# Optimization experiments

Hardware: AMD Instinct MI355X
Metric: run time of the kernel (lower is better)

Reference implementation:

```python
import jax, jax.numpy as jnp
import numpy as np

N_HEADS = 16
EMBED_DIM = 2048
BATCH, SEQ = 2, 2048


def setup_inputs() -> dict:
    key = jax.random.key(0)
    k1, k2, k3, k4, k5 = jax.random.split(key, 5)
    s_in = 1.0 / np.sqrt(EMBED_DIM)
    return {
        "x": jax.random.normal(k1, (BATCH, SEQ, EMBED_DIM), dtype=jnp.float32),
        "w_in": jax.random.normal(k2, (3 * EMBED_DIM, EMBED_DIM), dtype=jnp.float32) * s_in,
        "b_in": jax.random.normal(k3, (3 * EMBED_DIM,), dtype=jnp.float32) * 0.02,
        "w_out": jax.random.normal(k4, (EMBED_DIM, EMBED_DIM), dtype=jnp.float32) * s_in,
        "b_out": jax.random.normal(k5, (EMBED_DIM,), dtype=jnp.float32) * 0.02,
        "causal_mask": 1,
    }


def reference(x, w_in, b_in, w_out, b_out, causal_mask):
    b, l, e = x.shape
    h, d = N_HEADS, e // N_HEADS
    qkv = x @ w_in.T + b_in                      # [b, l, 3e]
    q, k, v = jnp.split(qkv, 3, axis=-1)
    # b l (h d) -> b h l d
    q = q.reshape(b, l, h, d).transpose(0, 2, 1, 3)
    k = k.reshape(b, l, h, d).transpose(0, 2, 1, 3)
    v = v.reshape(b, l, h, d).transpose(0, 2, 1, 3)
    scores = jnp.einsum("bhqd,bhkd->bhqk", q, k) / jnp.sqrt(jnp.float32(d))
    if causal_mask:
        tri = jnp.triu(jnp.ones((l, l), dtype=bool), k=1)  # True above diagonal
        scores = jnp.where(tri, -jnp.inf, scores)
    attn = jax.nn.softmax(scores, axis=-1)
    out = jnp.einsum("bhqk,bhkd->bhqd", attn, v)  # [b, h, l, d]
    out = out.transpose(0, 2, 1, 3).reshape(b, l, e)
    return out @ w_out.T + b_out
```

## Files before the change

### kernel.cpp

```cpp
#include <hip/hip_runtime.h>
#include <hip/hip_bf16.h>
#include <math.h>

typedef __attribute__((ext_vector_type(4))) float floatx4;
typedef __attribute__((ext_vector_type(16))) float floatx16;
typedef __attribute__((ext_vector_type(8))) __bf16 bf16x8;

__device__ __forceinline__ unsigned short f2bf(float f) {
    union { float f; unsigned int u; } v; v.f = f;
    unsigned int u = v.u;
    u += 0x7FFFu + ((u >> 16) & 1u);
    return (unsigned short)(u >> 16);
}

__device__ __forceinline__ unsigned int pkbf(float a, float b) {
    return (unsigned int)f2bf(a) | ((unsigned int)f2bf(b) << 16);
}

__device__ __forceinline__ void gl_lds16(const void* g, void* l) {
    __builtin_amdgcn_global_load_lds(
        (const __attribute__((address_space(1))) void*)g,
        (__attribute__((address_space(3))) void*)l, 16, 0, 0);
}

__global__ void cast_f32_bf16(const float* __restrict__ in,
                              unsigned short* __restrict__ out, int n) {
    int i = (blockIdx.x * blockDim.x + threadIdx.x) * 4;
    if (i + 4 <= n) {
        float4 f = *(const float4*)(in + i);
        ushort4 o;
        o.x = f2bf(f.x); o.y = f2bf(f.y); o.z = f2bf(f.z); o.w = f2bf(f.w);
        *(ushort4*)(out + i) = o;
    }
}


#define VMCNT(n) asm volatile("s_waitcnt vmcnt(" #n ")" ::: "memory")
#define LGKM0()  asm volatile("s_waitcnt lgkmcnt(0)" ::: "memory")
#define BARF()   do { asm volatile("" ::: "memory"); __builtin_amdgcn_s_barrier(); \
                      asm volatile("" ::: "memory"); } while (0)

#define STAGE_A4(bsel, tt, h) do { \
    const unsigned short* _s = Ab + (size_t)((h) * 128 + rstage) * K + (tt) * 64 + scol; \
    char* _d = bufc + (bsel) * 49152 + (h) * 16384 + wid * 1024; \
    gl_lds16(_s, _d); \
    gl_lds16(_s + (size_t)64 * K, _d + 8192); \
} while (0)

#define STAGE_B4(bsel, tt, h) do { \
    const unsigned short* _s = Bb + (size_t)((h) * 64 + rstage) * K + (tt) * 64 + scol; \
    char* _d = bufc + (bsel) * 49152 + 32768 + (h) * 8192 + wid * 1024; \
    gl_lds16(_s, _d); \
} while (0)

#define STAGE_TILE(bsel, tt) do { \
    STAGE_A4(bsel, tt, 0); STAGE_A4(bsel, tt, 1); \
    STAGE_B4(bsel, tt, 0); STAGE_B4(bsel, tt, 1); \
} while (0)

#define RDA(base, ii, kse) (*(const bf16x8*)((base) + (ii) * 2048 + rdoffA + (kse)))
#define RDB(base, jj, kse) (*(const bf16x8*)((base) + (jj) * 2048 + rdoffB + (kse)))

#define MFMA_C(iofs) do { \
    __builtin_amdgcn_s_setprio(1); \
    _Pragma("unroll") \
    for (int ii = 0; ii < 4; ++ii) { \
        _Pragma("unroll") \
        for (int jj = 0; jj < 2; ++jj) { \
            acc[(iofs) + ii][jj] = __builtin_amdgcn_mfma_f32_16x16x32_bf16( \
                aF[((iofs) + ii) * 2 + 0], bL[jj * 2 + 0], acc[(iofs) + ii][jj], 0, 0, 0); \
            acc[(iofs) + ii][jj] = __builtin_amdgcn_mfma_f32_16x16x32_bf16( \
                aF[((iofs) + ii) * 2 + 1], bL[jj * 2 + 1], acc[(iofs) + ii][jj], 0, 0, 0); \
        } } \
    __builtin_amdgcn_s_setprio(0); \
} while (0)

template<int MODE>
__global__ __launch_bounds__(512, 2) void gemm4p(
    const unsigned short* __restrict__ A,
    const unsigned short* __restrict__ B,
    const float* __restrict__ bias,
    float* __restrict__ Cf,
    unsigned short* __restrict__ q_ws,
    unsigned short* __restrict__ k_ws,
    unsigned short* __restrict__ vT_ws,
    int M, int N, int K)
{
    extern __shared__ char ldsc[];
    char* const bufc = ldsc;

    const int nby = M >> 8;
    const int nwg = gridDim.x;
    const int qq = nwg >> 3;
    const int wg = (blockIdx.x & 7) * qq + (blockIdx.x >> 3);
    const int by = wg % nby, bx = wg / nby;
    const int m0 = by << 8, n0 = bx << 7;

    const int tid = threadIdx.x;
    const int lane = tid & 63, wid = tid >> 6;
    const int li = lane & 15, quad = lane >> 4;
    const int wr = wid >> 2, wc = wid & 3;

    const int rstage = tid >> 3;
    const int scol = (((tid & 7) ^ ((tid >> 3) & 7)) << 3);
    const unsigned short* Ab = A + (size_t)m0 * K;
    const unsigned short* Bb = B + (size_t)n0 * K;

    const int swz = (lane & 7) << 4;
    const int ks0 = ((quad << 4)     ) ^ swz;
    const int ks1 = ((quad << 4) + 64) ^ swz;
    const int rdoffA = li * 128;
    const int rdoffB = li * 128 + ((wc & 1) << 12);

    const char* rdA0 = bufc + wr * 16384;
    const char* rdB0 = bufc + 32768 + (wc >> 1) * 8192;
    const char* rdA1 = rdA0 + 49152;
    const char* rdB1 = rdB0 + 49152;

    floatx4 acc[8][2] = {};
    bf16x8 aF[16], bL[4];

    const int KTn = K >> 6;

    STAGE_TILE(0, 0);
    STAGE_TILE(1, 1);
    VMCNT(6);
    BARF();

    for (int t = 0; t < KTn; t += 2) {
        const bool pf = (t + 2 < KTn);

        #pragma unroll
        for (int ii = 0; ii < 8; ++ii) { aF[ii*2+0] = RDA(rdA0, ii, ks0); aF[ii*2+1] = RDA(rdA0, ii, ks1); }
        #pragma unroll
        for (int jj = 0; jj < 2; ++jj) { bL[jj*2+0] = RDB(rdB0, jj, ks0); bL[jj*2+1] = RDB(rdB0, jj, ks1); }
        BARF();
        MFMA_C(0);
        LGKM0();
        BARF();

        if (pf) STAGE_TILE(0, t + 2);
        BARF();
        MFMA_C(4);
        if (pf) { VMCNT(6); } else { VMCNT(0); }
        BARF();

        #pragma unroll
        for (int ii = 0; ii < 8; ++ii) { aF[ii*2+0] = RDA(rdA1, ii, ks0); aF[ii*2+1] = RDA(rdA1, ii, ks1); }
        #pragma unroll
        for (int jj = 0; jj < 2; ++jj) { bL[jj*2+0] = RDB(rdB1, jj, ks0); bL[jj*2+1] = RDB(rdB1, jj, ks1); }
        BARF();
        MFMA_C(0);
        LGKM0();
        BARF();

        if (pf) STAGE_TILE(1, t + 3);
        BARF();
        MFMA_C(4);
        if (pf) { VMCNT(6); } else { VMCNT(0); }
        BARF();
    }

    const int colb = wc * 32;
    const int rowb = wr * 128;
    if (MODE == 0) {
        #pragma unroll
        for (int i2 = 0; i2 < 8; ++i2)
            #pragma unroll
            for (int j2 = 0; j2 < 2; ++j2) {
                const int col = n0 + colb + j2 * 16 + li;
                const float bv = bias[col];
                #pragma unroll
                for (int r = 0; r < 4; ++r) {
                    const int row = m0 + rowb + i2 * 16 + quad * 4 + r;
                    Cf[(size_t)row * N + col] = acc[i2][j2][r] + bv;
                }
            }
    } else {
        const int which = bx >> 4;
        const int hh = bx & 15;
        const int lbase = m0 & 2047;
        const size_t bh = (size_t)((m0 >> 11) * 16 + hh);
        if (which == 2) {
            unsigned short (*Lv)[264] = (unsigned short(*)[264])ldsc;
            #pragma unroll
            for (int i2 = 0; i2 < 8; ++i2)
                #pragma unroll
                for (int j2 = 0; j2 < 2; ++j2) {
                    const int col = colb + j2 * 16 + li;
                    const float bv = bias[n0 + col];
                    #pragma unroll
                    for (int r = 0; r < 4; ++r) {
                        const int row = rowb + i2 * 16 + quad * 4 + r;
                        Lv[col][row] = f2bf(acc[i2][j2][r] + bv);
                    }
                }
            __syncthreads();
            #pragma unroll
            for (int c = 0; c < 8; ++c) {
                int chunk = c * 512 + tid;
                int d = chunk >> 5;
                int ls = (chunk & 31) * 8;
                *(uint4*)(vT_ws + (bh * 128 + d) * 2048 + lbase + ls) =
                    *(const uint4*)&Lv[d][ls];
            }
        } else {
            unsigned short (*Lq)[136] = (unsigned short(*)[136])ldsc;
            #pragma unroll
            for (int i2 = 0; i2 < 8; ++i2)
                #pragma unroll
                for (int j2 = 0; j2 < 2; ++j2) {
                    const int col = colb + j2 * 16 + li;
                    const float bv = bias[n0 + col];
                    #pragma unroll
                    for (int r = 0; r < 4; ++r) {
                        const int row = rowb + i2 * 16 + quad * 4 + r;
                        Lq[row][col] = f2bf(acc[i2][j2][r] + bv);
                    }
                }
            __syncthreads();
            unsigned short* dst = which ? k_ws : q_ws;
            #pragma unroll
            for (int c = 0; c < 8; ++c) {
                int chunk = c * 512 + tid;
                int row = chunk >> 4;
                int dc = (chunk & 15) * 8;
                *(uint4*)(dst + (bh * 2048 + lbase + row) * (size_t)128 + dc) =
                    *(const uint4*)&Lq[row][dc];
            }
        }
    }
}

__global__ __launch_bounds__(256, 3) void attn_kernel(
    const unsigned short* __restrict__ q_ws,
    const unsigned short* __restrict__ k_ws,
    const unsigned short* __restrict__ vT_ws,
    unsigned short* __restrict__ aout,
    const int* __restrict__ causal_ptr)
{
    __shared__ unsigned short smem[64 * 136 + 128 * 72];
    unsigned short* const Ks = smem;
    unsigned short* const Vs = smem + 64 * 136;

    const int ord = blockIdx.x;
    int qt, bhid;
    if (ord < 256) { qt = ord >> 5;              bhid = ord & 31; }
    else           { qt = 15 - ((ord - 256) >> 5); bhid = ord & 31; }
    const int b = bhid >> 4, h = bhid & 15;

    const int tid = threadIdx.x;
    const int lane = tid & 63, w = tid >> 6;
    const int lq = lane & 31;
    const int half = lane >> 5;
    const size_t bh = (size_t)(b * 16 + h);
    const unsigned short* Qp = q_ws + bh * 2048 * 128;
    const unsigned short* Kp = k_ws + bh * 2048 * 128;
    const unsigned short* Vp = vT_ws + bh * 128 * 2048;
    const int causal = causal_ptr[0];
    const float scale = 0.08838834764831845f;

    const int qg = qt * 128 + w * 32 + lq;
    bf16x8 qf[8];
    #pragma unroll
    for (int s = 0; s < 8; ++s)
        qf[s] = *(const bf16x8*)(Qp + (size_t)qg * 128 + s * 16 + half * 8);

    floatx16 O[4] = {};
    float m_i = -INFINITY, l_i = 0.f;

    const int myEnd = causal ? (2 * qt + 1) : 31;
    for (int kt = 0; kt <= myEnd; ++kt) {
        #pragma unroll
        for (int c = 0; c < 4; ++c) {
            int chunk = c * 256 + tid;
            int krow = chunk >> 4;
            int kcc  = (chunk & 15) * 8;
            *(uint4*)(Ks + krow * 136 + kcc) =
                *(const uint4*)(Kp + (size_t)(kt * 64 + krow) * 128 + kcc);
            int vrow = chunk >> 3;
            int vcc  = (chunk & 7) * 8;
            *(uint4*)(Vs + vrow * 72 + vcc) =
                *(const uint4*)(Vp + (size_t)vrow * 2048 + kt * 64 + vcc);
        }
        __syncthreads();

        floatx16 S[2] = {};
        #pragma unroll
        for (int ct = 0; ct < 2; ++ct)
            #pragma unroll
            for (int s = 0; s < 8; ++s) {
                bf16x8 kf = *(const bf16x8*)(Ks + (ct * 32 + lq) * 136 + s * 16 + half * 8);
                S[ct] = __builtin_amdgcn_mfma_f32_32x32x16_bf16(kf, qf[s], S[ct], 0, 0, 0);
            }

        const bool diag = causal && (kt >= 2 * qt);
        float mx = -INFINITY;
        #pragma unroll
        for (int ct = 0; ct < 2; ++ct)
            #pragma unroll
            for (int r = 0; r < 16; ++r) {
                float sv = S[ct][r] * scale;
                if (diag) {
                    int key = kt * 64 + 32 * ct + (r & 3) + 8 * (r >> 2) + 4 * half;
                    if (key > qg) sv = -INFINITY;
                }
                S[ct][r] = sv;
                mx = fmaxf(mx, sv);
            }
        mx = fmaxf(mx, __shfl_xor(mx, 32, 64));
        float m_new = fmaxf(m_i, mx);
        float m_use = (m_new == -INFINITY) ? 0.f : m_new;
        float alpha = __expf(m_i - m_use);

        float rs = 0.f;
        #pragma unroll
        for (int ct = 0; ct < 2; ++ct)
            #pragma unroll
            for (int r = 0; r < 16; ++r) {
                float p = __expf(S[ct][r] - m_use);
                S[ct][r] = p;
                rs += p;
            }
        rs += __shfl_xor(rs, 32, 64);
        l_i = l_i * alpha + rs;
        m_i = m_new;
        #pragma unroll
        for (int dt = 0; dt < 4; ++dt)
            #pragma unroll
            for (int r = 0; r < 16; ++r)
                O[dt][r] *= alpha;

        bf16x8 pfr[4];
        #pragma unroll
        for (int ct = 0; ct < 2; ++ct)
            #pragma unroll
            for (int h2 = 0; h2 < 2; ++h2) {
                int base = 8 * h2;
                unsigned int pk0 = pkbf(S[ct][base + 0], S[ct][base + 1]);
                unsigned int pk1 = pkbf(S[ct][base + 2], S[ct][base + 3]);
                unsigned int pk2 = pkbf(S[ct][base + 4], S[ct][base + 5]);
                unsigned int pk3 = pkbf(S[ct][base + 6], S[ct][base + 7]);
                unsigned int x0 = __shfl_xor((int)pk0, 32, 64);
                unsigned int x1 = __shfl_xor((int)pk1, 32, 64);
                unsigned int x2 = __shfl_xor((int)pk2, 32, 64);
                unsigned int x3 = __shfl_xor((int)pk3, 32, 64);
                union { unsigned int u[4]; bf16x8 v; } fr;
                fr.u[0] = half ? x2 : pk0;
                fr.u[1] = half ? x3 : pk1;
                fr.u[2] = half ? pk2 : x0;
                fr.u[3] = half ? pk3 : x1;
                pfr[ct * 2 + h2] = fr.v;
            }

        #pragma unroll
        for (int dt = 0; dt < 4; ++dt)
            #pragma unroll
            for (int s = 0; s < 4; ++s) {
                bf16x8 vf = *(const bf16x8*)(Vs + (dt * 32 + lq) * 72 + s * 16 + half * 8);
                O[dt] = __builtin_amdgcn_mfma_f32_32x32x16_bf16(vf, pfr[s], O[dt], 0, 0, 0);
            }
        __syncthreads();
    }

    unsigned short* const Ep = smem;
    const float invl = 1.0f / l_i;
    #pragma unroll
    for (int dt = 0; dt < 4; ++dt)
        #pragma unroll
        for (int g = 0; g < 4; ++g) {
            int dbase = dt * 32 + g * 8 + half * 4;
            ushort4 o4;
            o4.x = f2bf(O[dt][g * 4 + 0] * invl);
            o4.y = f2bf(O[dt][g * 4 + 1] * invl);
            o4.z = f2bf(O[dt][g * 4 + 2] * invl);
            o4.w = f2bf(O[dt][g * 4 + 3] * invl);
            *(ushort4*)(Ep + (w * 32 + lq) * 136 + dbase) = o4;
        }
    __syncthreads();
    #pragma unroll
    for (int c = 0; c < 8; ++c) {
        int chunk = c * 256 + tid;
        int row = chunk >> 4;
        int dc = (chunk & 15) * 8;
        uint4 v = *(const uint4*)(Ep + row * 136 + dc);
        *(uint4*)(aout + ((size_t)b * 2048 + qt * 128 + row) * 2048 + h * 128 + dc) = v;
    }
}

extern "C" void kernel_launch(void* const* d_in, const int* in_sizes, int n_in,
                              void* d_out, int out_size, void* d_ws, size_t ws_size,
                              hipStream_t stream) {
    const float* x     = (const float*)d_in[0];
    const float* w_in  = (const float*)d_in[1];
    const float* b_in  = (const float*)d_in[2];
    const float* w_out = (const float*)d_in[3];
    const float* b_out = (const float*)d_in[4];
    const int* causal  = (const int*)d_in[5];

    char* ws = (char*)d_ws;
    unsigned short* xb    = (unsigned short*)ws; ws += (size_t)4096 * 2048 * 2;
    unsigned short* wb    = (unsigned short*)ws; ws += (size_t)6144 * 2048 * 2;
    unsigned short* wob   = (unsigned short*)ws; ws += (size_t)2048 * 2048 * 2;
    unsigned short* q_ws  = (unsigned short*)ws; ws += (size_t)32 * 2048 * 128 * 2;
    unsigned short* k_ws  = (unsigned short*)ws; ws += (size_t)32 * 2048 * 128 * 2;
    unsigned short* vT_ws = (unsigned short*)ws; ws += (size_t)32 * 2048 * 128 * 2;
    unsigned short* aout  = (unsigned short*)ws; ws += (size_t)4096 * 2048 * 2;

    static int once = []() {
        auto* f0 = gemm4p<0>;
        auto* f1 = gemm4p<1>;
        hipFuncSetAttribute((const void*)f0,
            hipFuncAttributeMaxDynamicSharedMemorySize, 98304);
        hipFuncSetAttribute((const void*)f1,
            hipFuncAttributeMaxDynamicSharedMemorySize, 98304);
        return 0;
    }();
    (void)once;

    cast_f32_bf16<<<8192, 256, 0, stream>>>(x, xb, 4096 * 2048);
    cast_f32_bf16<<<12288, 256, 0, stream>>>(w_in, wb, 6144 * 2048);
    cast_f32_bf16<<<4096, 256, 0, stream>>>(w_out, wob, 2048 * 2048);

    gemm4p<1><<<768, 512, 98304, stream>>>(
        xb, wb, b_in, nullptr, q_ws, k_ws, vT_ws, 4096, 6144, 2048);

    attn_kernel<<<512, 256, 0, stream>>>(
        q_ws, k_ws, vT_ws, aout, causal);

    gemm4p<0><<<256, 512, 98304, stream>>>(
        aout, wob, b_out, (float*)d_out, nullptr, nullptr, nullptr,
        4096, 2048, 2048);
}
```

Measured before the change: 467.5 us.

## Split attention keys across warps with 64-row query tiles and merge partial softmax

The query tile per block shrinks from 128 to 64 rows, doubling the grid to 1024 blocks. The four warps now form a 2x2 split: two handle query halves and two handle key halves of each 64-key tile. The two key-split partial results are merged through shared memory with a log-sum-exp combine before the bf16 store. Block order now goes from longest causal tile first, and launch bounds move from 3 to 4 blocks per CU to raise occupancy and balance the causal workload. The cost is an extra epilogue reduction, an fp32 staging buffer, and K/V tiles reloaded for half as many queries each.

Measured after the change: 521.4 us. 1.12x slower.

```diff
diff --git a/kernel.cpp b/kernel.cpp
--- a/kernel.cpp
+++ b/kernel.cpp
@@ -232,7 +232,7 @@
     }
 }
 
-__global__ __launch_bounds__(256, 3) void attn_kernel(
+__global__ __launch_bounds__(256, 4) void attn_kernel(
     const unsigned short* __restrict__ q_ws,
     const unsigned short* __restrict__ k_ws,
     const unsigned short* __restrict__ vT_ws,
@@ -244,13 +244,13 @@
     unsigned short* const Vs = smem + 64 * 136;
 
     const int ord = blockIdx.x;
-    int qt, bhid;
-    if (ord < 256) { qt = ord >> 5;              bhid = ord & 31; }
-    else           { qt = 15 - ((ord - 256) >> 5); bhid = ord & 31; }
+    const int bhid = ord >> 5;
+    const int qt = 31 - (ord & 31);
     const int b = bhid >> 4, h = bhid & 15;
 
     const int tid = threadIdx.x;
     const int lane = tid & 63, w = tid >> 6;
+    const int wq = w & 1, wk = w >> 1;
     const int lq = lane & 31;
     const int half = lane >> 5;
     const size_t bh = (size_t)(b * 16 + h);
@@ -260,7 +260,7 @@
     const int causal = causal_ptr[0];
     const float scale = 0.08838834764831845f;
 
-    const int qg = qt * 128 + w * 32 + lq;
+    const int qg = qt * 64 + wq * 32 + lq;
     bf16x8 qf[8];
     #pragma unroll
     for (int s = 0; s < 8; ++s)
@@ -269,8 +269,8 @@
     floatx16 O[4] = {};
     float m_i = -INFINITY, l_i = 0.f;
 
-    const int myEnd = causal ? (2 * qt + 1) : 31;
-    for (int kt = 0; kt <= myEnd; ++kt) {
+    const int nkt = causal ? (qt + 1) : 32;
+    for (int kt = 0; kt < nkt; ++kt) {
         #pragma unroll
         for (int c = 0; c < 4; ++c) {
             int chunk = c * 256 + tid;
@@ -285,29 +285,25 @@
         }
         __syncthreads();
 
-        floatx16 S[2] = {};
-        #pragma unroll
-        for (int ct = 0; ct < 2; ++ct)
-            #pragma unroll
-            for (int s = 0; s < 8; ++s) {
-                bf16x8 kf = *(const bf16x8*)(Ks + (ct * 32 + lq) * 136 + s * 16 + half * 8);
-                S[ct] = __builtin_amdgcn_mfma_f32_32x32x16_bf16(kf, qf[s], S[ct], 0, 0, 0);
-            }
-
-        const bool diag = causal && (kt >= 2 * qt);
+        floatx16 S = {};
+        #pragma unroll
+        for (int s = 0; s < 8; ++s) {
+            bf16x8 kf = *(const bf16x8*)(Ks + (wk * 32 + lq) * 136 + s * 16 + half * 8);
+            S = __builtin_amdgcn_mfma_f32_32x32x16_bf16(kf, qf[s], S, 0, 0, 0);
+        }
+
+        const bool diag = causal && (kt == qt);
         float mx = -INFINITY;
         #pragma unroll
-        for (int ct = 0; ct < 2; ++ct)
-            #pragma unroll
-            for (int r = 0; r < 16; ++r) {
-                float sv = S[ct][r] * scale;
-                if (diag) {
-                    int key = kt * 64 + 32 * ct + (r & 3) + 8 * (r >> 2) + 4 * half;
-                    if (key > qg) sv = -INFINITY;
-                }
-                S[ct][r] = sv;
-                mx = fmaxf(mx, sv);
-            }
+        for (int r = 0; r < 16; ++r) {
+            float sv = S[r] * scale;
+            if (diag) {
+                int key = kt * 64 + wk * 32 + (r & 3) + 8 * (r >> 2) + 4 * half;
+                if (key > qg) sv = -INFINITY;
+            }
+            S[r] = sv;
+            mx = fmaxf(mx, sv);
+        }
         mx = fmaxf(mx, __shfl_xor(mx, 32, 64));
         float m_new = fmaxf(m_i, mx);
         float m_use = (m_new == -INFINITY) ? 0.f : m_new;
@@ -315,13 +311,11 @@
 
         float rs = 0.f;
         #pragma unroll
-        for (int ct = 0; ct < 2; ++ct)
-            #pragma unroll
-            for (int r = 0; r < 16; ++r) {
-                float p = __expf(S[ct][r] - m_use);
-                S[ct][r] = p;
-                rs += p;
-            }
+        for (int r = 0; r < 16; ++r) {
+            float p = __expf(S[r] - m_use);
+            S[r] = p;
+            rs += p;
+        }
         rs += __shfl_xor(rs, 32, 64);
         l_i = l_i * alpha + rs;
         m_i = m_new;
@@ -331,60 +325,84 @@
             for (int r = 0; r < 16; ++r)
                 O[dt][r] *= alpha;
 
-        bf16x8 pfr[4];
-        #pragma unroll
-        for (int ct = 0; ct < 2; ++ct)
-            #pragma unroll
-            for (int h2 = 0; h2 < 2; ++h2) {
-                int base = 8 * h2;
-                unsigned int pk0 = pkbf(S[ct][base + 0], S[ct][base + 1]);
-                unsigned int pk1 = pkbf(S[ct][base + 2], S[ct][base + 3]);
-                unsigned int pk2 = pkbf(S[ct][base + 4], S[ct][base + 5]);
-                unsigned int pk3 = pkbf(S[ct][base + 6], S[ct][base + 7]);
-                unsigned int x0 = __shfl_xor((int)pk0, 32, 64);
-                unsigned int x1 = __shfl_xor((int)pk1, 32, 64);
-                unsigned int x2 = __shfl_xor((int)pk2, 32, 64);
-                unsigned int x3 = __shfl_xor((int)pk3, 32, 64);
-                union { unsigned int u[4]; bf16x8 v; } fr;
-                fr.u[0] = half ? x2 : pk0;
-                fr.u[1] = half ? x3 : pk1;
-                fr.u[2] = half ? pk2 : x0;
-                fr.u[3] = half ? pk3 : x1;
-                pfr[ct * 2 + h2] = fr.v;
-            }
+        bf16x8 pfr[2];
+        #pragma unroll
+        for (int h2 = 0; h2 < 2; ++h2) {
+            int base = 8 * h2;
+            unsigned int pk0 = pkbf(S[base + 0], S[base + 1]);
+            unsigned int pk1 = pkbf(S[base + 2], S[base + 3]);
+            unsigned int pk2 = pkbf(S[base + 4], S[base + 5]);
+            unsigned int pk3 = pkbf(S[base + 6], S[base + 7]);
+            unsigned int x0 = __shfl_xor((int)pk0, 32, 64);
+            unsigned int x1 = __shfl_xor((int)pk1, 32, 64);
+            unsigned int x2 = __shfl_xor((int)pk2, 32, 64);
+            unsigned int x3 = __shfl_xor((int)pk3, 32, 64);
+            union { unsigned int u[4]; bf16x8 v; } fr;
+            fr.u[0] = half ? x2 : pk0;
+            fr.u[1] = half ? x3 : pk1;
+            fr.u[2] = half ? pk2 : x0;
+            fr.u[3] = half ? pk3 : x1;
+            pfr[h2] = fr.v;
+        }
 
         #pragma unroll
         for (int dt = 0; dt < 4; ++dt)
             #pragma unroll
-            for (int s = 0; s < 4; ++s) {
-                bf16x8 vf = *(const bf16x8*)(Vs + (dt * 32 + lq) * 72 + s * 16 + half * 8);
+            for (int s = 0; s < 2; ++s) {
+                bf16x8 vf = *(const bf16x8*)(Vs + (dt * 32 + lq) * 72 + wk * 32 + s * 16 + half * 8);
                 O[dt] = __builtin_amdgcn_mfma_f32_32x32x16_bf16(vf, pfr[s], O[dt], 0, 0, 0);
             }
         __syncthreads();
     }
 
-    unsigned short* const Ep = smem;
-    const float invl = 1.0f / l_i;
+    float* const Ep  = (float*)smem;
+    float* const stm = (float*)smem + 64 * 132;
+    float* const stl = stm + 128;
+    if (lane < 32) {
+        stm[(wk * 2 + wq) * 32 + lq] = m_i;
+        stl[(wk * 2 + wq) * 32 + lq] = l_i;
+    }
+    __syncthreads();
+    const float m_o = stm[((wk ^ 1) * 2 + wq) * 32 + lq];
+    const float l_o = stl[((wk ^ 1) * 2 + wq) * 32 + lq];
+    const float M = fmaxf(m_i, m_o);
+    const float sc  = __expf(m_i - M);
+    const float l_f = l_i * sc + l_o * __expf(m_o - M);
+    const float f = sc / l_f;
+
+    if (wk == 0) {
+        #pragma unroll
+        for (int dt = 0; dt < 4; ++dt)
+            #pragma unroll
+            for (int r = 0; r < 16; ++r) {
+                int d = dt * 32 + (r & 3) + 8 * (r >> 2) + 4 * half;
+                Ep[(wq * 32 + lq) * 132 + d] = O[dt][r] * f;
+            }
+    }
+    __syncthreads();
+    if (wk == 1) {
+        #pragma unroll
+        for (int dt = 0; dt < 4; ++dt)
+            #pragma unroll
+            for (int r = 0; r < 16; ++r) {
+                int d = dt * 32 + (r & 3) + 8 * (r >> 2) + 4 * half;
+                Ep[(wq * 32 + lq) * 132 + d] += O[dt][r] * f;
+            }
+    }
+    __syncthreads();
+
     #pragma unroll
-    for (int dt = 0; dt < 4; ++dt)
-        #pragma unroll
-        for (int g = 0; g < 4; ++g) {
-            int dbase = dt * 32 + g * 8 + half * 4;
-            ushort4 o4;
-            o4.x = f2bf(O[dt][g * 4 + 0] * invl);
-            o4.y = f2bf(O[dt][g * 4 + 1] * invl);
-            o4.z = f2bf(O[dt][g * 4 + 2] * invl);
-            o4.w = f2bf(O[dt][g * 4 + 3] * invl);
-            *(ushort4*)(Ep + (w * 32 + lq) * 136 + dbase) = o4;
-        }
-    __syncthreads();
-    #pragma unroll
-    for (int c = 0; c < 8; ++c) {
+    for (int c = 0; c < 4; ++c) {
         int chunk = c * 256 + tid;
         int row = chunk >> 4;
         int dc = (chunk & 15) * 8;
-        uint4 v = *(const uint4*)(Ep + row * 136 + dc);
-        *(uint4*)(aout + ((size_t)b * 2048 + qt * 128 + row) * 2048 + h * 128 + dc) = v;
+        const float* ep = Ep + row * 132 + dc;
+        ushort4 o0, o1;
+        o0.x = f2bf(ep[0]); o0.y = f2bf(ep[1]); o0.z = f2bf(ep[2]); o0.w = f2bf(ep[3]);
+        o1.x = f2bf(ep[4]); o1.y = f2bf(ep[5]); o1.z = f2bf(ep[6]); o1.w = f2bf(ep[7]);
+        unsigned short* dst = aout + ((size_t)b * 2048 + qt * 64 + row) * 2048 + h * 128 + dc;
+        *(ushort4*)dst = o0;
+        *(ushort4*)(dst + 4) = o1;
     }
 }
 
@@ -425,7 +443,7 @@
     gemm4p<1><<<768, 512, 98304, stream>>>(
         xb, wb, b_in, nullptr, q_ws, k_ws, vT_ws, 4096, 6144, 2048);
 
-    attn_kernel<<<512, 256, 0, stream>>>(
+    attn_kernel<<<1024, 256, 0, stream>>>(
         q_ws, k_ws, vT_ws, aout, causal);
 
     gemm4p<0><<<256, 512, 98304, stream>>>(
```
